# Kernel optimization log

Hardware: AMD Instinct MI355X
Metric: run time of the kernel (lower is better)

The kernel has to match this reference:

```python
import jax, jax.numpy as jnp
import numpy as np

B, NQ, N, D_IN, D_KEY, D_MODEL = 8, 2048, 2048, 512, 512, 512


def setup_inputs() -> dict:
    key = jax.random.key(0)
    k1, k2, k3, k4, k5, k6 = jax.random.split(key, 6)
    lim_k = np.sqrt(6.0 / (D_IN + D_KEY))
    lim_v = np.sqrt(6.0 / (D_IN + D_MODEL))
    return {
        "node_features": jax.random.normal(k1, (B, N, D_IN), dtype=jnp.float32),
        "query": jax.random.normal(k2, (B, NQ, D_IN), dtype=jnp.float32),
        "mask": jax.random.bernoulli(k3, 0.3, (NQ, B, N)),  # True = masked out
        "wq": jax.random.uniform(k4, (D_IN, D_KEY), jnp.float32, -lim_k, lim_k),
        "wk": jax.random.uniform(k5, (D_IN, D_KEY), jnp.float32, -lim_k, lim_k),
        "wv": jax.random.uniform(k6, (D_IN, D_MODEL), jnp.float32, -lim_v, lim_v),
    }


def reference(node_features, query, mask, wq, wk, wv):
    # Projections
    Q = query @ wq              # [B, NQ, d_key]
    K = node_features @ wk      # [B, N, d_key]
    V = node_features @ wv      # [B, N, d_model]
    # Raw scores [B, NQ, N]
    scores = jnp.einsum("bqd,bnd->bqn", Q, K)
    b, nq, n = scores.shape
    # Faithful to tf: reshape to (NQ, B, N), mask with float32.min, reshape back
    s = scores.reshape(nq, b, n)
    masked = jnp.where(mask, jnp.finfo(jnp.float32).min, s).reshape(b, nq, n)
    # Scale AFTER masking (as in the original), then softmax over keys
    attn = jax.nn.softmax(masked / jnp.sqrt(jnp.float32(K.shape[-1])), axis=-1)
    return attn @ V             # [B, NQ, d_model]
```

## Files before the change

kernel.cpp:

```cpp
#include <hip/hip_runtime.h>

typedef __attribute__((ext_vector_type(8))) short bf16x8;
typedef __attribute__((ext_vector_type(4))) float f32x4;

__device__ __forceinline__ unsigned short f2bf(float f) {
  unsigned int u = __builtin_bit_cast(unsigned int, f);
  u += 0x7fffu + ((u >> 16) & 1u);
  return (unsigned short)(u >> 16);
}

#define GLD16(gp, lp) __builtin_amdgcn_global_load_lds( \
    (const __attribute__((address_space(1))) unsigned int*)(gp), \
    (__attribute__((address_space(3))) unsigned int*)(lp), 16, 0, 0)

__global__ void detect_mode(const unsigned int* __restrict__ mask, int* __restrict__ flag) {
  __shared__ int c1s;
  if (threadIdx.x == 0) c1s = 0;
  __syncthreads();
  int c1 = 0;
  for (int i = threadIdx.x; i < 16384; i += 256) {
    unsigned int u = mask[i];
    if (u & 0x0000ff00u) c1++;
  }
  atomicAdd(&c1s, c1);
  __syncthreads();
  if (threadIdx.x == 0) *flag = (c1s > 0) ? 1 : 4;
}

__global__ __launch_bounds__(256) void pack_mask(
    const unsigned char* __restrict__ m, const int* __restrict__ flag,
    unsigned long long* __restrict__ pm)
{
  const int g = blockIdx.x * 256 + threadIdx.x;
  const size_t base = (size_t)g * 64;
  unsigned long long bits = 0;
  if (*flag == 1) {
    const uint4* p = (const uint4*)(m + base);
#pragma unroll
    for (int j = 0; j < 4; ++j) {
      uint4 v = p[j];
      unsigned int w[4] = {v.x, v.y, v.z, v.w};
#pragma unroll
      for (int q = 0; q < 4; ++q) {
        unsigned int u = w[q];
#pragma unroll
        for (int b = 0; b < 4; ++b)
          if ((u >> (8 * b)) & 0xffu) bits |= 1ull << (j * 16 + q * 4 + b);
      }
    }
  } else {
    const uint4* p = (const uint4*)(m + base * 4);
#pragma unroll
    for (int j = 0; j < 16; ++j) {
      uint4 v = p[j];
      if (v.x) bits |= 1ull << (j * 4 + 0);
      if (v.y) bits |= 1ull << (j * 4 + 1);
      if (v.z) bits |= 1ull << (j * 4 + 2);
      if (v.w) bits |= 1ull << (j * 4 + 3);
    }
  }
  pm[g] = bits;
}

__global__ void cvt_two(const float* __restrict__ a, const float* __restrict__ b,
                        unsigned short* __restrict__ oa, unsigned short* __restrict__ ob) {
  int i = blockIdx.x * 256 + threadIdx.x;
  const float* src;
  unsigned short* dst;
  int j;
  if (i < 2097152) { src = a; dst = oa; j = i; }
  else             { src = b; dst = ob; j = i - 2097152; }
  float4 v = ((const float4*)src)[j];
  ushort4 o;
  o.x = f2bf(v.x); o.y = f2bf(v.y); o.z = f2bf(v.z); o.w = f2bf(v.w);
  ((ushort4*)dst)[j] = o;
}

__global__ void cvt_w3(const float* __restrict__ wq, const float* __restrict__ wk,
                       const float* __restrict__ wv,
                       unsigned short* __restrict__ oq, unsigned short* __restrict__ ok,
                       unsigned short* __restrict__ ov) {
  int idx = blockIdx.x * 256 + threadIdx.x;
  int w = idx >> 18;
  int rem = idx & 262143;
  int n = rem >> 9, k = rem & 511;
  const float* W = (w == 0) ? wq : (w == 1) ? wk : wv;
  unsigned short* O = (w == 0) ? oq : (w == 1) ? ok : ov;
  O[n * 512 + k] = f2bf(W[k * 512 + n]);
}

__global__ __launch_bounds__(512, 1) void gemm256_scores(
    const unsigned short* __restrict__ Qg, const unsigned short* __restrict__ Kg,
    unsigned short* __restrict__ Sg, const unsigned long long* __restrict__ pm,
    float* __restrict__ sums)
{
  extern __shared__ char smem[];
  const long z = blockIdx.z;
  const unsigned short* Ab = Qg + z * 1048576;
  const unsigned short* Bb = Kg + z * 1048576;
  unsigned short* C = Sg + z * 4194304;
  const unsigned long long* pmask = pm + z * 65536;
  float* sumz = sums + z * 2048;
  const long bm = (long)blockIdx.x * 256;
  const long bn = (long)blockIdx.y * 256;

  const int tid = threadIdx.x;
  const int lane = tid & 63;
  const int wid = tid >> 6;
  const int wr = wid >> 1;
  const int wc = wid & 1;
  const int fr = lane & 15, fq = lane >> 4;
  const int srow = tid >> 3;
  const int clog = (tid & 7) ^ (srow & 7);

  char* buf0 = smem;
  char* buf1 = smem + 65536;

  f32x4 acc[4][8] = {};

  const int swz0 = ((fq)     ^ (fr & 7)) * 16;
  const int swz1 = ((4 + fq) ^ (fr & 7)) * 16;
  const int arow = (wr * 64 + fr) * 128;
  const int brow = (wc * 128 + fr) * 128;

  {
    const unsigned short* ga = Ab + (bm + srow) * 512 + clog * 8;
    const unsigned short* gb = Bb + (bn + srow) * 512 + clog * 8;
#pragma unroll
    for (int l = 0; l < 4; ++l) {
      GLD16(ga + (long)l * 64 * 512, buf0 + l * 8192 + tid * 16);
      GLD16(gb + (long)l * 64 * 512, buf0 + 32768 + l * 8192 + tid * 16);
    }
  }

  char* cur = buf0;
  char* nxt = buf1;
  for (int t = 0; t < 8; ++t) {
    __builtin_amdgcn_sched_barrier(0);
    __builtin_amdgcn_s_barrier();
    if (t < 7) {
      const long k0 = (long)(t + 1) * 64;
      const unsigned short* ga = Ab + (bm + srow) * 512 + k0 + clog * 8;
      const unsigned short* gb = Bb + (bn + srow) * 512 + k0 + clog * 8;
#pragma unroll
      for (int l = 0; l < 4; ++l) {
        GLD16(ga + (long)l * 64 * 512, nxt + l * 8192 + tid * 16);
        GLD16(gb + (long)l * 64 * 512, nxt + 32768 + l * 8192 + tid * 16);
      }
      asm volatile("s_waitcnt vmcnt(8)" ::: "memory");
    } else {
      asm volatile("s_waitcnt vmcnt(0)" ::: "memory");
    }
    __builtin_amdgcn_s_barrier();
    __builtin_amdgcn_sched_barrier(0);

    const char* bufA = cur;
    const char* bufB = cur + 32768;
#pragma unroll
    for (int kh = 0; kh < 2; ++kh) {
      const int swz = kh ? swz1 : swz0;
      bf16x8 a[4];
#pragma unroll
      for (int mi = 0; mi < 4; ++mi)
        a[mi] = *(const bf16x8*)(bufA + arow + mi * 2048 + swz);
#pragma unroll
      for (int nh = 0; nh < 2; ++nh) {
        bf16x8 b[4];
#pragma unroll
        for (int nj = 0; nj < 4; ++nj)
          b[nj] = *(const bf16x8*)(bufB + brow + (nh * 4 + nj) * 2048 + swz);
        __builtin_amdgcn_sched_barrier(0);
        __builtin_amdgcn_s_barrier();
        __builtin_amdgcn_s_setprio(1);
#pragma unroll
        for (int mi = 0; mi < 4; ++mi)
#pragma unroll
          for (int nj = 0; nj < 4; ++nj)
            acc[mi][nh * 4 + nj] = __builtin_amdgcn_mfma_f32_16x16x32_bf16(
                a[mi], b[nj], acc[mi][nh * 4 + nj], 0, 0, 0);
        __builtin_amdgcn_s_setprio(0);
        __builtin_amdgcn_sched_barrier(0);
      }
    }
    char* tmp = cur; cur = nxt; nxt = tmp;
  }

  const float SCALE = 0.04419417382415922f;
  const long wbase = (bn >> 6) + wc * 2;
#pragma unroll
  for (int mi = 0; mi < 4; ++mi) {
    const long rowb = bm + wr * 64 + mi * 16 + fq * 4;
#pragma unroll
    for (int r = 0; r < 4; ++r) {
      const long row = rowb + r;
      const unsigned long long w0 = pmask[row * 32 + wbase];
      const unsigned long long w1 = pmask[row * 32 + wbase + 1];
      unsigned short* Crow = C + row * 2048 + bn + wc * 128 + fr;
      float s = 0.f;
#pragma unroll
      for (int ni = 0; ni < 8; ++ni) {
        const unsigned long long w = (ni < 4) ? w0 : w1;
        const int sh = (ni & 3) * 16 + fr;
        float e = ((w >> sh) & 1ull) ? 0.0f : __expf(acc[mi][ni][r] * SCALE);
        s += e;
        Crow[ni * 16] = f2bf(e);
      }
      s += __shfl_xor(s, 1); s += __shfl_xor(s, 2);
      s += __shfl_xor(s, 4); s += __shfl_xor(s, 8);
      if (fr == 0) atomicAdd(&sumz[row], s);
    }
  }
}

__device__ __forceinline__ void gemm_narrow_core(
    const unsigned short* __restrict__ Ab,
    const unsigned short* __restrict__ Bb,
    void* __restrict__ Cb,
    long ldA, long ldB, long ldO, int nk, long bm, long bn, char* smem,
    int mode, const float* __restrict__ sumz)
{
  const int tid = threadIdx.x;
  const int lane = tid & 63;
  const int wid = tid >> 6;
  const int wr = wid >> 1;
  const int wc = wid & 1;
  const int fr = lane & 15, fq = lane >> 4;
  const int srow = tid >> 3;
  const int clog = (tid & 7) ^ (srow & 7);

  char* buf0 = smem;
  char* buf1 = smem + 49152;

  f32x4 acc[4][4] = {};

  const int swz0 = ((fq)     ^ (fr & 7)) * 16;
  const int swz1 = ((4 + fq) ^ (fr & 7)) * 16;
  const int arow = (wr * 64 + fr) * 128;
  const int brow = (wc * 64 + fr) * 128;

  {
    const unsigned short* ga = Ab + (bm + srow) * ldA + clog * 8;
    const unsigned short* gb = Bb + (bn + srow) * ldB + clog * 8;
#pragma unroll
    for (int l = 0; l < 4; ++l)
      GLD16(ga + (long)l * 64 * ldA, buf0 + l * 8192 + tid * 16);
#pragma unroll
    for (int l = 0; l < 2; ++l)
      GLD16(gb + (long)l * 64 * ldB, buf0 + 32768 + l * 8192 + tid * 16);
  }

  char* cur = buf0;
  char* nxt = buf1;
  for (int t = 0; t < nk; ++t) {
    __builtin_amdgcn_sched_barrier(0);
    __builtin_amdgcn_s_barrier();
    if (t + 1 < nk) {
      const long k0 = (long)(t + 1) * 64;
      const unsigned short* ga = Ab + (bm + srow) * ldA + k0 + clog * 8;
      const unsigned short* gb = Bb + (bn + srow) * ldB + k0 + clog * 8;
#pragma unroll
      for (int l = 0; l < 4; ++l)
        GLD16(ga + (long)l * 64 * ldA, nxt + l * 8192 + tid * 16);
#pragma unroll
      for (int l = 0; l < 2; ++l)
        GLD16(gb + (long)l * 64 * ldB, nxt + 32768 + l * 8192 + tid * 16);
      asm volatile("s_waitcnt vmcnt(6)" ::: "memory");
    } else {
      asm volatile("s_waitcnt vmcnt(0)" ::: "memory");
    }
    __builtin_amdgcn_s_barrier();
    __builtin_amdgcn_sched_barrier(0);

    const char* bufA = cur;
    const char* bufB = cur + 32768;
#pragma unroll
    for (int kh = 0; kh < 2; ++kh) {
      const int swz = kh ? swz1 : swz0;
      bf16x8 a[4], b[4];
#pragma unroll
      for (int mi = 0; mi < 4; ++mi)
        a[mi] = *(const bf16x8*)(bufA + arow + mi * 2048 + swz);
#pragma unroll
      for (int nj = 0; nj < 4; ++nj)
        b[nj] = *(const bf16x8*)(bufB + brow + nj * 2048 + swz);
      __builtin_amdgcn_sched_barrier(0);
      __builtin_amdgcn_s_barrier();
      __builtin_amdgcn_s_setprio(1);
#pragma unroll
      for (int mi = 0; mi < 4; ++mi)
#pragma unroll
        for (int nj = 0; nj < 4; ++nj)
          acc[mi][nj] = __builtin_amdgcn_mfma_f32_16x16x32_bf16(
              a[mi], b[nj], acc[mi][nj], 0, 0, 0);
      __builtin_amdgcn_s_setprio(0);
      __builtin_amdgcn_sched_barrier(0);
    }
    char* tmp = cur; cur = nxt; nxt = tmp;
  }

  if (mode == 0) {
    unsigned short* C = (unsigned short*)Cb;
#pragma unroll
    for (int mi = 0; mi < 4; ++mi)
#pragma unroll
      for (int nj = 0; nj < 4; ++nj) {
        const long row = bm + wr * 64 + mi * 16 + fq * 4;
        const long col = bn + wc * 64 + nj * 16 + fr;
#pragma unroll
        for (int r = 0; r < 4; ++r)
          C[(row + r) * ldO + col] = f2bf(acc[mi][nj][r]);
      }
  } else {
    float* C = (float*)Cb;
#pragma unroll
    for (int mi = 0; mi < 4; ++mi) {
      const long rowb = bm + wr * 64 + mi * 16 + fq * 4;
#pragma unroll
      for (int r = 0; r < 4; ++r) {
        const long row = rowb + r;
        const float iv = 1.0f / sumz[row];
        const long colb = bn + wc * 64 + fr;
#pragma unroll
        for (int nj = 0; nj < 4; ++nj)
          C[row * ldO + colb + nj * 16] = acc[mi][nj][r] * iv;
      }
    }
  }
}

__global__ __launch_bounds__(512, 1) void gemm_proj(
    const unsigned short* __restrict__ Xq, const unsigned short* __restrict__ Xn,
    const unsigned short* __restrict__ Wqt, const unsigned short* __restrict__ Wkt,
    const unsigned short* __restrict__ Wvt,
    unsigned short* __restrict__ Q, unsigned short* __restrict__ Kb,
    unsigned short* __restrict__ Vt)
{
  extern __shared__ char smem[];
  const int z = blockIdx.z;
  if (z == 0) {
    gemm_narrow_core(Xq, Wqt, Q, 512, 512, 512, 8,
                     (long)blockIdx.x * 256, (long)blockIdx.y * 128, smem, 0, nullptr);
  } else if (z == 1) {
    gemm_narrow_core(Xn, Wkt, Kb, 512, 512, 512, 8,
                     (long)blockIdx.x * 256, (long)blockIdx.y * 128, smem, 0, nullptr);
  } else {
    const int flat = blockIdx.x * 4 + blockIdx.y;
    gemm_narrow_core(Wvt, Xn, Vt, 512, 512, 16384, 8,
                     (long)(flat >> 7) * 256, (long)(flat & 127) * 128, smem, 0, nullptr);
  }
}

__global__ __launch_bounds__(512, 1) void gemm_pv(
    const unsigned short* __restrict__ E, const unsigned short* __restrict__ Vt,
    const float* __restrict__ sums, float* __restrict__ O)
{
  extern __shared__ char smem[];
  const long z = blockIdx.z;
  gemm_narrow_core(E + z * 4194304, Vt + z * 2048, O + z * 1048576,
                   2048, 16384, 512, 32,
                   (long)blockIdx.x * 256, (long)blockIdx.y * 128, smem,
                   1, sums + z * 2048);
}

extern "C" void kernel_launch(void* const* d_in, const int* in_sizes, int n_in,
                              void* d_out, int out_size, void* d_ws, size_t ws_size,
                              hipStream_t stream) {
  const float* node  = (const float*)d_in[0];
  const float* query = (const float*)d_in[1];
  const unsigned char* mask = (const unsigned char*)d_in[2];
  const float* wq = (const float*)d_in[3];
  const float* wk = (const float*)d_in[4];
  const float* wv = (const float*)d_in[5];
  float* out = (float*)d_out;

  char* ws = (char*)d_ws;
  unsigned short* Q   = (unsigned short*)(ws);
  unsigned short* Kb  = (unsigned short*)(ws + 16777216);
  unsigned short* Vt  = (unsigned short*)(ws + 33554432);
  unsigned short* E   = (unsigned short*)(ws + 50331648);
  unsigned short* Xq  = (unsigned short*)(ws + 50331648);
  unsigned short* Xn  = (unsigned short*)(ws + 50331648 + 16777216);
  unsigned short* Wqt = (unsigned short*)(ws + 50331648 + 33554432);
  unsigned short* Wkt = Wqt + 262144;
  unsigned short* Wvt = Wkt + 262144;
  float* sums = (float*)(ws + 117440512);
  int* flag   = (int*)(ws + 117506048);
  unsigned long long* pm = (unsigned long long*)(ws + 118489088);

  detect_mode<<<1, 256, 0, stream>>>((const unsigned int*)mask, flag);
  pack_mask<<<2048, 256, 0, stream>>>(mask, flag, pm);

  cvt_two<<<16384, 256, 0, stream>>>(query, node, Xq, Xn);
  cvt_w3<<<3072, 256, 0, stream>>>(wq, wk, wv, Wqt, Wkt, Wvt);

  dim3 gp(64, 4, 3);
  gemm_proj<<<gp, 512, 98304, stream>>>(Xq, Xn, Wqt, Wkt, Wvt, Q, Kb, Vt);

  hipMemsetAsync(sums, 0, 65536, stream);
  dim3 gs(8, 8, 8);
  gemm256_scores<<<gs, 512, 131072, stream>>>(Q, Kb, E, pm, sums);

  dim3 gv(8, 4, 8);
  gemm_pv<<<gv, 512, 98304, stream>>>(E, Vt, sums, out);
}
```

Before: 219.1 us.

## Replace big-tile GEMMs with 128x128 triple-buffered core at higher occupancy

All three GEMM stages (projections, scores with mask+exp epilogue, PV) now share one 128x128 tile core with 256 threads, K-step of 32, and a three-stage LDS pipeline. Launch bounds allow three blocks per CU, so smaller tiles give more blocks and more waves in flight, hiding latency. The cost is lower per-block data reuse and more global and LDS traffic per FLOP. It also adds more atomic row-sum updates in the scores epilogue.

```diff
diff --git a/kernel.cpp b/kernel.cpp
--- a/kernel.cpp
+++ b/kernel.cpp
@@ -89,215 +89,83 @@
   O[n * 512 + k] = f2bf(W[k * 512 + n]);
 }
 
-__global__ __launch_bounds__(512, 1) void gemm256_scores(
-    const unsigned short* __restrict__ Qg, const unsigned short* __restrict__ Kg,
-    unsigned short* __restrict__ Sg, const unsigned long long* __restrict__ pm,
-    float* __restrict__ sums)
-{
-  extern __shared__ char smem[];
-  const long z = blockIdx.z;
-  const unsigned short* Ab = Qg + z * 1048576;
-  const unsigned short* Bb = Kg + z * 1048576;
-  unsigned short* C = Sg + z * 4194304;
-  const unsigned long long* pmask = pm + z * 65536;
-  float* sumz = sums + z * 2048;
-  const long bm = (long)blockIdx.x * 256;
-  const long bn = (long)blockIdx.y * 256;
-
+__device__ __forceinline__ void core128(
+    const unsigned short* __restrict__ Ab, const unsigned short* __restrict__ Bb,
+    void* __restrict__ Cb, long ldA, long ldB, long ldO, int nk,
+    long bm, long bn, char* smem, int mode,
+    const unsigned long long* __restrict__ pmask, float* __restrict__ sumz,
+    const float* __restrict__ sums_ro)
+{
   const int tid = threadIdx.x;
   const int lane = tid & 63;
   const int wid = tid >> 6;
-  const int wr = wid >> 1;
-  const int wc = wid & 1;
+  const int wr = wid >> 1, wc = wid & 1;
   const int fr = lane & 15, fq = lane >> 4;
-  const int srow = tid >> 3;
-  const int clog = (tid & 7) ^ (srow & 7);
-
-  char* buf0 = smem;
-  char* buf1 = smem + 65536;
-
-  f32x4 acc[4][8] = {};
-
-  const int swz0 = ((fq)     ^ (fr & 7)) * 16;
-  const int swz1 = ((4 + fq) ^ (fr & 7)) * 16;
-  const int arow = (wr * 64 + fr) * 128;
-  const int brow = (wc * 128 + fr) * 128;
-
-  {
-    const unsigned short* ga = Ab + (bm + srow) * 512 + clog * 8;
-    const unsigned short* gb = Bb + (bn + srow) * 512 + clog * 8;
-#pragma unroll
-    for (int l = 0; l < 4; ++l) {
-      GLD16(ga + (long)l * 64 * 512, buf0 + l * 8192 + tid * 16);
-      GLD16(gb + (long)l * 64 * 512, buf0 + 32768 + l * 8192 + tid * 16);
-    }
-  }
-
-  char* cur = buf0;
-  char* nxt = buf1;
-  for (int t = 0; t < 8; ++t) {
-    __builtin_amdgcn_sched_barrier(0);
-    __builtin_amdgcn_s_barrier();
-    if (t < 7) {
-      const long k0 = (long)(t + 1) * 64;
-      const unsigned short* ga = Ab + (bm + srow) * 512 + k0 + clog * 8;
-      const unsigned short* gb = Bb + (bn + srow) * 512 + k0 + clog * 8;
-#pragma unroll
-      for (int l = 0; l < 4; ++l) {
-        GLD16(ga + (long)l * 64 * 512, nxt + l * 8192 + tid * 16);
-        GLD16(gb + (long)l * 64 * 512, nxt + 32768 + l * 8192 + tid * 16);
-      }
-      asm volatile("s_waitcnt vmcnt(8)" ::: "memory");
-    } else {
-      asm volatile("s_waitcnt vmcnt(0)" ::: "memory");
-    }
-    __builtin_amdgcn_s_barrier();
-    __builtin_amdgcn_sched_barrier(0);
-
-    const char* bufA = cur;
-    const char* bufB = cur + 32768;
-#pragma unroll
-    for (int kh = 0; kh < 2; ++kh) {
-      const int swz = kh ? swz1 : swz0;
-      bf16x8 a[4];
-#pragma unroll
-      for (int mi = 0; mi < 4; ++mi)
-        a[mi] = *(const bf16x8*)(bufA + arow + mi * 2048 + swz);
-#pragma unroll
-      for (int nh = 0; nh < 2; ++nh) {
-        bf16x8 b[4];
-#pragma unroll
-        for (int nj = 0; nj < 4; ++nj)
-          b[nj] = *(const bf16x8*)(bufB + brow + (nh * 4 + nj) * 2048 + swz);
-        __builtin_amdgcn_sched_barrier(0);
-        __builtin_amdgcn_s_barrier();
-        __builtin_amdgcn_s_setprio(1);
-#pragma unroll
-        for (int mi = 0; mi < 4; ++mi)
-#pragma unroll
-          for (int nj = 0; nj < 4; ++nj)
-            acc[mi][nh * 4 + nj] = __builtin_amdgcn_mfma_f32_16x16x32_bf16(
-                a[mi], b[nj], acc[mi][nh * 4 + nj], 0, 0, 0);
-        __builtin_amdgcn_s_setprio(0);
-        __builtin_amdgcn_sched_barrier(0);
-      }
-    }
-    char* tmp = cur; cur = nxt; nxt = tmp;
-  }
-
-  const float SCALE = 0.04419417382415922f;
-  const long wbase = (bn >> 6) + wc * 2;
-#pragma unroll
-  for (int mi = 0; mi < 4; ++mi) {
-    const long rowb = bm + wr * 64 + mi * 16 + fq * 4;
-#pragma unroll
-    for (int r = 0; r < 4; ++r) {
-      const long row = rowb + r;
-      const unsigned long long w0 = pmask[row * 32 + wbase];
-      const unsigned long long w1 = pmask[row * 32 + wbase + 1];
-      unsigned short* Crow = C + row * 2048 + bn + wc * 128 + fr;
-      float s = 0.f;
-#pragma unroll
-      for (int ni = 0; ni < 8; ++ni) {
-        const unsigned long long w = (ni < 4) ? w0 : w1;
-        const int sh = (ni & 3) * 16 + fr;
-        float e = ((w >> sh) & 1ull) ? 0.0f : __expf(acc[mi][ni][r] * SCALE);
-        s += e;
-        Crow[ni * 16] = f2bf(e);
-      }
-      s += __shfl_xor(s, 1); s += __shfl_xor(s, 2);
-      s += __shfl_xor(s, 4); s += __shfl_xor(s, 8);
-      if (fr == 0) atomicAdd(&sumz[row], s);
-    }
-  }
-}
-
-__device__ __forceinline__ void gemm_narrow_core(
-    const unsigned short* __restrict__ Ab,
-    const unsigned short* __restrict__ Bb,
-    void* __restrict__ Cb,
-    long ldA, long ldB, long ldO, int nk, long bm, long bn, char* smem,
-    int mode, const float* __restrict__ sumz)
-{
-  const int tid = threadIdx.x;
-  const int lane = tid & 63;
-  const int wid = tid >> 6;
-  const int wr = wid >> 1;
-  const int wc = wid & 1;
-  const int fr = lane & 15, fq = lane >> 4;
-  const int srow = tid >> 3;
-  const int clog = (tid & 7) ^ (srow & 7);
-
-  char* buf0 = smem;
-  char* buf1 = smem + 49152;
+
+  char* b0 = smem;
+  char* b1 = smem + 16384;
+  char* b2 = smem + 32768;
+
+  const int s0 = tid, s1 = tid + 256;
+  const int r0 = s0 >> 2, c0 = (s0 & 3) ^ ((r0 ^ (r0 >> 2)) & 3);
+  const int r1 = s1 >> 2, c1 = (s1 & 3) ^ ((r1 ^ (r1 >> 2)) & 3);
+
+#define STAGE(buf, kt) do { \
+    const long k0_ = (long)(kt) << 5; \
+    GLD16(Ab + (bm + r0) * ldA + k0_ + c0 * 8, (buf) + tid * 16); \
+    GLD16(Ab + (bm + r1) * ldA + k0_ + c1 * 8, (buf) + 4096 + tid * 16); \
+    GLD16(Bb + (bn + r0) * ldB + k0_ + c0 * 8, (buf) + 8192 + tid * 16); \
+    GLD16(Bb + (bn + r1) * ldB + k0_ + c1 * 8, (buf) + 12288 + tid * 16); \
+  } while (0)
+
+  int aoff[4], boff[4];
+#pragma unroll
+  for (int i = 0; i < 4; ++i) {
+    const int ra = wr * 64 + i * 16 + fr;
+    aoff[i] = ra * 64 + (fq ^ ((ra ^ (ra >> 2)) & 3)) * 16;
+    const int rb = wc * 64 + i * 16 + fr;
+    boff[i] = 8192 + rb * 64 + (fq ^ ((rb ^ (rb >> 2)) & 3)) * 16;
+  }
 
   f32x4 acc[4][4] = {};
 
-  const int swz0 = ((fq)     ^ (fr & 7)) * 16;
-  const int swz1 = ((4 + fq) ^ (fr & 7)) * 16;
-  const int arow = (wr * 64 + fr) * 128;
-  const int brow = (wc * 64 + fr) * 128;
-
-  {
-    const unsigned short* ga = Ab + (bm + srow) * ldA + clog * 8;
-    const unsigned short* gb = Bb + (bn + srow) * ldB + clog * 8;
-#pragma unroll
-    for (int l = 0; l < 4; ++l)
-      GLD16(ga + (long)l * 64 * ldA, buf0 + l * 8192 + tid * 16);
-#pragma unroll
-    for (int l = 0; l < 2; ++l)
-      GLD16(gb + (long)l * 64 * ldB, buf0 + 32768 + l * 8192 + tid * 16);
-  }
-
-  char* cur = buf0;
-  char* nxt = buf1;
+  STAGE(b0, 0);
+  STAGE(b1, 1);
+  char* cur = b0; char* nx1 = b1; char* nx2 = b2;
+
   for (int t = 0; t < nk; ++t) {
     __builtin_amdgcn_sched_barrier(0);
     __builtin_amdgcn_s_barrier();
-    if (t + 1 < nk) {
-      const long k0 = (long)(t + 1) * 64;
-      const unsigned short* ga = Ab + (bm + srow) * ldA + k0 + clog * 8;
-      const unsigned short* gb = Bb + (bn + srow) * ldB + k0 + clog * 8;
-#pragma unroll
-      for (int l = 0; l < 4; ++l)
-        GLD16(ga + (long)l * 64 * ldA, nxt + l * 8192 + tid * 16);
-#pragma unroll
-      for (int l = 0; l < 2; ++l)
-        GLD16(gb + (long)l * 64 * ldB, nxt + 32768 + l * 8192 + tid * 16);
-      asm volatile("s_waitcnt vmcnt(6)" ::: "memory");
+    if (t + 2 < nk) {
+      STAGE(nx2, t + 2);
+      asm volatile("s_waitcnt vmcnt(8)" ::: "memory");
+    } else if (t + 1 < nk) {
+      asm volatile("s_waitcnt vmcnt(4)" ::: "memory");
     } else {
       asm volatile("s_waitcnt vmcnt(0)" ::: "memory");
     }
     __builtin_amdgcn_s_barrier();
     __builtin_amdgcn_sched_barrier(0);
 
-    const char* bufA = cur;
-    const char* bufB = cur + 32768;
-#pragma unroll
-    for (int kh = 0; kh < 2; ++kh) {
-      const int swz = kh ? swz1 : swz0;
-      bf16x8 a[4], b[4];
+    bf16x8 a[4];
+#pragma unroll
+    for (int mi = 0; mi < 4; ++mi)
+      a[mi] = *(const bf16x8*)(cur + aoff[mi]);
+    __builtin_amdgcn_s_setprio(1);
+#pragma unroll
+    for (int nj = 0; nj < 4; ++nj) {
+      const bf16x8 b = *(const bf16x8*)(cur + boff[nj]);
 #pragma unroll
       for (int mi = 0; mi < 4; ++mi)
-        a[mi] = *(const bf16x8*)(bufA + arow + mi * 2048 + swz);
-#pragma unroll
-      for (int nj = 0; nj < 4; ++nj)
-        b[nj] = *(const bf16x8*)(bufB + brow + nj * 2048 + swz);
-      __builtin_amdgcn_sched_barrier(0);
-      __builtin_amdgcn_s_barrier();
-      __builtin_amdgcn_s_setprio(1);
-#pragma unroll
-      for (int mi = 0; mi < 4; ++mi)
-#pragma unroll
-        for (int nj = 0; nj < 4; ++nj)
-          acc[mi][nj] = __builtin_amdgcn_mfma_f32_16x16x32_bf16(
-              a[mi], b[nj], acc[mi][nj], 0, 0, 0);
-      __builtin_amdgcn_s_setprio(0);
-      __builtin_amdgcn_sched_barrier(0);
-    }
-    char* tmp = cur; cur = nxt; nxt = tmp;
-  }
-
+        acc[mi][nj] = __builtin_amdgcn_mfma_f32_16x16x32_bf16(a[mi], b, acc[mi][nj], 0, 0, 0);
+    }
+    __builtin_amdgcn_s_setprio(0);
+
+    char* tmp = cur; cur = nx1; nx1 = nx2; nx2 = tmp;
+  }
+#undef STAGE
+
+  const float SCALE = 0.04419417382415922f;
   if (mode == 0) {
     unsigned short* C = (unsigned short*)Cb;
 #pragma unroll
@@ -310,6 +178,30 @@
         for (int r = 0; r < 4; ++r)
           C[(row + r) * ldO + col] = f2bf(acc[mi][nj][r]);
       }
+  } else if (mode == 1) {
+    unsigned short* C = (unsigned short*)Cb;
+    const long wword = (bn >> 6) + wc;
+#pragma unroll
+    for (int mi = 0; mi < 4; ++mi) {
+      const long rowb = bm + wr * 64 + mi * 16 + fq * 4;
+#pragma unroll
+      for (int r = 0; r < 4; ++r) {
+        const long row = rowb + r;
+        const unsigned long long w = pmask[row * 32 + wword];
+        unsigned short* Crow = C + row * ldO + bn + wc * 64 + fr;
+        float s = 0.f;
+#pragma unroll
+        for (int nj = 0; nj < 4; ++nj) {
+          const int sh = nj * 16 + fr;
+          float e = ((w >> sh) & 1ull) ? 0.0f : __expf(acc[mi][nj][r] * SCALE);
+          s += e;
+          Crow[nj * 16] = f2bf(e);
+        }
+        s += __shfl_xor(s, 1); s += __shfl_xor(s, 2);
+        s += __shfl_xor(s, 4); s += __shfl_xor(s, 8);
+        if (fr == 0) atomicAdd(&sumz[row], s);
+      }
+    }
   } else {
     float* C = (float*)Cb;
 #pragma unroll
@@ -318,7 +210,7 @@
 #pragma unroll
       for (int r = 0; r < 4; ++r) {
         const long row = rowb + r;
-        const float iv = 1.0f / sumz[row];
+        const float iv = 1.0f / sums_ro[row];
         const long colb = bn + wc * 64 + fr;
 #pragma unroll
         for (int nj = 0; nj < 4; ++nj)
@@ -328,7 +220,7 @@
   }
 }
 
-__global__ __launch_bounds__(512, 1) void gemm_proj(
+__global__ __launch_bounds__(256, 3) void gemm_proj(
     const unsigned short* __restrict__ Xq, const unsigned short* __restrict__ Xn,
     const unsigned short* __restrict__ Wqt, const unsigned short* __restrict__ Wkt,
     const unsigned short* __restrict__ Wvt,
@@ -338,28 +230,39 @@
   extern __shared__ char smem[];
   const int z = blockIdx.z;
   if (z == 0) {
-    gemm_narrow_core(Xq, Wqt, Q, 512, 512, 512, 8,
-                     (long)blockIdx.x * 256, (long)blockIdx.y * 128, smem, 0, nullptr);
+    core128(Xq, Wqt, Q, 512, 512, 512, 16,
+            (long)blockIdx.x * 128, (long)blockIdx.y * 128, smem, 0, nullptr, nullptr, nullptr);
   } else if (z == 1) {
-    gemm_narrow_core(Xn, Wkt, Kb, 512, 512, 512, 8,
-                     (long)blockIdx.x * 256, (long)blockIdx.y * 128, smem, 0, nullptr);
+    core128(Xn, Wkt, Kb, 512, 512, 512, 16,
+            (long)blockIdx.x * 128, (long)blockIdx.y * 128, smem, 0, nullptr, nullptr, nullptr);
   } else {
     const int flat = blockIdx.x * 4 + blockIdx.y;
-    gemm_narrow_core(Wvt, Xn, Vt, 512, 512, 16384, 8,
-                     (long)(flat >> 7) * 256, (long)(flat & 127) * 128, smem, 0, nullptr);
-  }
-}
-
-__global__ __launch_bounds__(512, 1) void gemm_pv(
+    core128(Wvt, Xn, Vt, 512, 512, 16384, 16,
+            (long)(flat >> 7) * 128, (long)(flat & 127) * 128, smem, 0, nullptr, nullptr, nullptr);
+  }
+}
+
+__global__ __launch_bounds__(256, 3) void gemm_scores(
+    const unsigned short* __restrict__ Q, const unsigned short* __restrict__ Kb,
+    unsigned short* __restrict__ E, const unsigned long long* __restrict__ pm,
+    float* __restrict__ sums)
+{
+  extern __shared__ char smem[];
+  const long z = blockIdx.z;
+  core128(Q + z * 1048576, Kb + z * 1048576, E + z * 4194304,
+          512, 512, 2048, 16, (long)blockIdx.x * 128, (long)blockIdx.y * 128, smem,
+          1, pm + z * 65536, sums + z * 2048, nullptr);
+}
+
+__global__ __launch_bounds__(256, 3) void gemm_pv(
     const unsigned short* __restrict__ E, const unsigned short* __restrict__ Vt,
     const float* __restrict__ sums, float* __restrict__ O)
 {
   extern __shared__ char smem[];
   const long z = blockIdx.z;
-  gemm_narrow_core(E + z * 4194304, Vt + z * 2048, O + z * 1048576,
-                   2048, 16384, 512, 32,
-                   (long)blockIdx.x * 256, (long)blockIdx.y * 128, smem,
-                   1, sums + z * 2048);
+  core128(E + z * 4194304, Vt + z * 2048, O + z * 1048576,
+          2048, 16384, 512, 64, (long)blockIdx.x * 128, (long)blockIdx.y * 128, smem,
+          2, nullptr, nullptr, sums + z * 2048);
 }
 
 extern "C" void kernel_launch(void* const* d_in, const int* in_sizes, int n_in,
@@ -393,13 +296,13 @@
   cvt_two<<<16384, 256, 0, stream>>>(query, node, Xq, Xn);
   cvt_w3<<<3072, 256, 0, stream>>>(wq, wk, wv, Wqt, Wkt, Wvt);
 
-  dim3 gp(64, 4, 3);
-  gemm_proj<<<gp, 512, 98304, stream>>>(Xq, Xn, Wqt, Wkt, Wvt, Q, Kb, Vt);
+  dim3 gp(128, 4, 3);
+  gemm_proj<<<gp, 256, 49152, stream>>>(Xq, Xn, Wqt, Wkt, Wvt, Q, Kb, Vt);
 
   hipMemsetAsync(sums, 0, 65536, stream);
-  dim3 gs(8, 8, 8);
-  gemm256_scores<<<gs, 512, 131072, stream>>>(Q, Kb, E, pm, sums);
-
-  dim3 gv(8, 4, 8);
-  gemm_pv<<<gv, 512, 98304, stream>>>(E, Vt, sums, out);
-}
+  dim3 gs(16, 16, 8);
+  gemm_scores<<<gs, 256, 49152, stream>>>(Q, Kb, E, pm, sums);
+
+  dim3 gv(16, 4, 8);
+  gemm_pv<<<gv, 256, 49152, stream>>>(E, Vt, sums, out);
+}
```

New measurement: 231.0 us. 1.05x slower.
